# Performance work log

Hardware: AMD Instinct MI355X
Metric: run time of the kernel (lower is better)

## Reference

```python
import jax, jax.numpy as jnp
import numpy as np

EPS = 1e-5
KC = 256  # key_channels


def conv1x1(x, w):
    # x: [N,Cin,H,W], w: [Cout,Cin] -> [N,Cout,H,W]
    return jnp.einsum('nchw,oc->nohw', x, w)


def bn_relu(x, g, b, m, v):
    # eval-mode BatchNorm2d + ReLU, fused affine form
    inv = g / jnp.sqrt(v + EPS)
    return jax.nn.relu(x * inv[None, :, None, None] + (b - m * inv)[None, :, None, None])


def setup_inputs() -> dict:
    key = jax.random.key(0)
    ks = jax.random.split(key, 8)
    N, C, H, W, K = 8, 512, 128, 128, 19
    d = {
        'x': jax.random.normal(ks[0], (N, C, H, W), jnp.float32),
        'proxy': jax.random.normal(ks[1], (N, C, K, 1), jnp.float32),
        'w_p1': jax.random.normal(ks[2], (KC, C), jnp.float32) / np.sqrt(C),
        'w_p2': jax.random.normal(ks[3], (KC, KC), jnp.float32) / np.sqrt(KC),
        'w_o1': jax.random.normal(ks[4], (KC, C), jnp.float32) / np.sqrt(C),
        'w_o2': jax.random.normal(ks[5], (KC, KC), jnp.float32) / np.sqrt(KC),
        'w_d': jax.random.normal(ks[6], (KC, C), jnp.float32) / np.sqrt(C),
        'w_u': jax.random.normal(ks[7], (C, KC), jnp.float32) / np.sqrt(KC),
    }
    for pfx, ch in [('p1', KC), ('p2', KC), ('o1', KC), ('o2', KC), ('d', KC), ('u', C)]:
        d[f'{pfx}_g'] = jnp.ones((ch,), jnp.float32)
        d[f'{pfx}_b'] = jnp.zeros((ch,), jnp.float32)
        d[f'{pfx}_m'] = jnp.zeros((ch,), jnp.float32)
        d[f'{pfx}_v'] = jnp.ones((ch,), jnp.float32)
    return d


def reference(x, proxy, w_p1, p1_g, p1_b, p1_m, p1_v, w_p2, p2_g, p2_b, p2_m, p2_v,
              w_o1, o1_g, o1_b, o1_m, o1_v, w_o2, o2_g, o2_b, o2_m, o2_v,
              w_d, d_g, d_b, d_m, d_v, w_u, u_g, u_b, u_m, u_v):
    N, C, H, W = x.shape
    # f_pixel: conv1x1 -> BN+ReLU -> conv1x1 -> BN+ReLU
    q = bn_relu(conv1x1(bn_relu(conv1x1(x, w_p1), p1_g, p1_b, p1_m, p1_v), w_p2),
                p2_g, p2_b, p2_m, p2_v)                       # [N,KC,H,W]
    k = bn_relu(conv1x1(bn_relu(conv1x1(proxy, w_o1), o1_g, o1_b, o1_m, o1_v), w_o2),
                o2_g, o2_b, o2_m, o2_v)                       # [N,KC,K,1]
    v = bn_relu(conv1x1(proxy, w_d), d_g, d_b, d_m, d_v)      # [N,KC,K,1]

    query = q.reshape(N, KC, H * W).transpose(0, 2, 1)        # [N,HW,KC]
    keym = k.reshape(N, KC, -1)                               # [N,KC,K]
    value = v.reshape(N, KC, -1).transpose(0, 2, 1)           # [N,K,KC]

    sim = jnp.einsum('nlc,nck->nlk', query, keym) * (KC ** -0.5)  # [N,HW,K]
    sim = jax.nn.softmax(sim, axis=-1)
    context = jnp.einsum('nlk,nkc->nlc', sim, value)          # [N,HW,KC]
    context = context.transpose(0, 2, 1).reshape(N, KC, H, W)
    # f_up
    return bn_relu(conv1x1(context, w_u), u_g, u_b, u_m, u_v)  # [N,C,H,W]
```

## Files before the change

kernel.cpp:

```cpp
#include <hip/hip_runtime.h>

#define HW     16384
#define CIN    512
#define KCH    256
#define NKEY   19
#define NKP    32
#define NBATCH 8

typedef __attribute__((ext_vector_type(8))) short s16x8;
typedef __attribute__((ext_vector_type(4))) short s16x4;
typedef __attribute__((ext_vector_type(4))) float f32x4;

__device__ __forceinline__ short f2bf(float f) {
  __bf16 h = (__bf16)f;
  return __builtin_bit_cast(short, h);
}

__global__ __launch_bounds__(256) void kprepA(
    const float* __restrict__ proxy,
    const float* __restrict__ w_p1, const float* __restrict__ w_p2,
    const float* __restrict__ p1g, const float* __restrict__ p1b,
    const float* __restrict__ p1m, const float* __restrict__ p1v,
    const float* __restrict__ p2g, const float* __restrict__ p2b,
    const float* __restrict__ p2m, const float* __restrict__ p2v,
    const float* __restrict__ ug,  const float* __restrict__ ub,
    const float* __restrict__ um,  const float* __restrict__ uvv,
    const float* __restrict__ w_o1, const float* __restrict__ w_d,
    const float* __restrict__ o1g, const float* __restrict__ o1b,
    const float* __restrict__ o1m, const float* __restrict__ o1v,
    const float* __restrict__ dg,  const float* __restrict__ db,
    const float* __restrict__ dm,  const float* __restrict__ dv,
    short* __restrict__ W1L, short* __restrict__ W2L,
    float* __restrict__ b1, float* __restrict__ b2, float* __restrict__ bu,
    float* __restrict__ t_o1g, float* __restrict__ vmatg)
{
  __shared__ char PB[32 * 1024];
  const int tid = threadIdx.x;
  if (blockIdx.x < 772) {
    int t = blockIdx.x * 256 + tid;
    if (t < 131072) {
      int kf = t >> 13, rem = t & 8191, tt = rem >> 9, e512 = rem & 511;
      int l = e512 >> 3, e = e512 & 7;
      int m = tt * 16 + (l & 15);
      int kcol = kf * 32 + (l >> 4) * 8 + e;
      float inv = p1g[m] * rsqrtf(p1v[m] + 1e-5f);
      W1L[t] = f2bf(inv * w_p1[(size_t)m * CIN + kcol]);
    } else if (t < 196608) {
      int u = t - 131072;
      int kf = u >> 13, rem = u & 8191, tt = rem >> 9, e512 = rem & 511;
      int l = e512 >> 3, e = e512 & 7;
      int m = tt * 16 + (l & 15);
      int kcol = kf * 32 + (l >> 4) * 8 + e;
      float inv = p2g[m] * rsqrtf(p2v[m] + 1e-5f);
      W2L[u] = f2bf(inv * w_p2[(size_t)m * KCH + kcol]);
    } else if (t < 196608 + 256) {
      int o = t - 196608;
      float inv = p1g[o] * rsqrtf(p1v[o] + 1e-5f);
      b1[o] = p1b[o] - p1m[o] * inv;
    } else if (t < 196608 + 512) {
      int o = t - 196608 - 256;
      float inv = p2g[o] * rsqrtf(p2v[o] + 1e-5f);
      b2[o] = p2b[o] - p2m[o] * inv;
    } else if (t < 196608 + 1024) {
      int o = t - 196608 - 512;
      float inv = ug[o] * rsqrtf(uvv[o] + 1e-5f);
      bu[o] = ub[o] - um[o] * inv;
    }
    return;
  }
  int bid = blockIdx.x - 772;
  int sel = bid >> 5;
  int r5  = bid & 31;
  int n   = r5 >> 2;
  int mbase = (r5 & 3) << 6;

  for (int j = 0; j < 8; ++j) *(s16x8*)(PB + (tid + j * 256) * 16) = (s16x8)0;
  __syncthreads();
  const float* pn = proxy + (size_t)n * CIN * NKEY;
  for (int e = tid; e < CIN * NKEY; e += 256) {
    int c = e / NKEY, k = e - c * NKEY;
    *(short*)(PB + k * 1024 + ((c << 1) ^ ((k & 7) << 4))) = f2bf(pn[e]);
  }
  __syncthreads();

  const int w = tid >> 6, lane = tid & 63, g = lane >> 4, i = lane & 15;
  const float* W  = sel ? w_d : w_o1;
  const float* gg = sel ? dg : o1g;
  const float* bb = sel ? db : o1b;
  const float* mm = sel ? dm : o1m;
  const float* vv = sel ? dv : o1v;
  f32x4 acc2[2];
  acc2[0] = (f32x4)0.f; acc2[1] = (f32x4)0.f;
  const int arow = mbase + w * 16 + i;
#pragma unroll 1
  for (int kf = 0; kf < 16; ++kf) {
    const float* wp = W + (size_t)arow * CIN + kf * 32 + g * 8;
    f32x4 a0 = *(const f32x4*)wp, a1 = *(const f32x4*)(wp + 4);
    s16x8 af;
#pragma unroll
    for (int e = 0; e < 4; ++e) { af[e] = f2bf(a0[e]); af[e + 4] = f2bf(a1[e]); }
#pragma unroll
    for (int nj = 0; nj < 2; ++nj) {
      int key = nj * 16 + i;
      s16x8 bf = *(const s16x8*)(PB + key * 1024 + ((kf * 64 + g * 16) ^ ((key & 7) << 4)));
      acc2[nj] = __builtin_amdgcn_mfma_f32_16x16x32_bf16(af, bf, acc2[nj], 0, 0, 0);
    }
  }
  float* dst = (sel ? vmatg : t_o1g) + (size_t)n * 8192;
#pragma unroll
  for (int r = 0; r < 4; ++r) {
    int o = mbase + w * 16 + g * 4 + r;
    float inv = gg[o] * rsqrtf(vv[o] + 1e-5f);
    float beta = bb[o] - mm[o] * inv;
#pragma unroll
    for (int nj = 0; nj < 2; ++nj) {
      int key = nj * 16 + i;
      dst[key * 256 + o] = fmaxf(acc2[nj][r] * inv + beta, 0.f);
    }
  }
}

__global__ __launch_bounds__(256) void kprepB(
    const float* __restrict__ w_o2, const float* __restrict__ w_u,
    const float* __restrict__ o2g, const float* __restrict__ o2b,
    const float* __restrict__ o2m, const float* __restrict__ o2v,
    const float* __restrict__ ug,  const float* __restrict__ uvv,
    const float* __restrict__ t_o1g, const float* __restrict__ vmatg,
    short* __restrict__ KmL, short* __restrict__ WuL)
{
  __shared__ char TB[32 * 512];
  const int tid = threadIdx.x;
  const int isKm = (blockIdx.x < 32);
  int n, mbase;
  const float* src;
  if (isKm) { n = blockIdx.x >> 2; mbase = (blockIdx.x & 3) << 6; src = t_o1g; }
  else { int b2_ = blockIdx.x - 32; n = b2_ >> 3; mbase = (b2_ & 7) << 6; src = vmatg; }
  const float* sn = src + (size_t)n * 8192;
  for (int j = 0; j < 32; ++j) {
    int idx = tid + j * 256;
    int key = idx >> 8, o = idx & 255;
    *(short*)(TB + key * 512 + ((o << 1) ^ ((key & 7) << 4))) = f2bf(sn[idx]);
  }
  __syncthreads();

  const int w = tid >> 6, lane = tid & 63, g = lane >> 4, i = lane & 15;
  const float* W = isKm ? w_o2 : w_u;
  f32x4 acc2[2];
  acc2[0] = (f32x4)0.f; acc2[1] = (f32x4)0.f;
  const int arow = mbase + w * 16 + i;
#pragma unroll 1
  for (int kf = 0; kf < 8; ++kf) {
    const float* wp = W + (size_t)arow * KCH + kf * 32 + g * 8;
    f32x4 a0 = *(const f32x4*)wp, a1 = *(const f32x4*)(wp + 4);
    s16x8 af;
#pragma unroll
    for (int e = 0; e < 4; ++e) { af[e] = f2bf(a0[e]); af[e + 4] = f2bf(a1[e]); }
#pragma unroll
    for (int nj = 0; nj < 2; ++nj) {
      int key = nj * 16 + i;
      s16x8 bf = *(const s16x8*)(TB + key * 512 + ((kf * 64 + g * 16) ^ ((key & 7) << 4)));
      acc2[nj] = __builtin_amdgcn_mfma_f32_16x16x32_bf16(af, bf, acc2[nj], 0, 0, 0);
    }
  }
  if (isKm) {
    short* Kn = KmL + (size_t)n * 8192;
#pragma unroll
    for (int r = 0; r < 4; ++r) {
      int o2 = mbase + w * 16 + g * 4 + r;
      float inv = o2g[o2] * rsqrtf(o2v[o2] + 1e-5f);
      float beta = o2b[o2] - o2m[o2] * inv;
#pragma unroll
      for (int nj = 0; nj < 2; ++nj) {
        float val = fmaxf(acc2[nj][r] * inv + beta, 0.f) * 0.0625f;
        Kn[((o2 >> 5) * 2 + nj) * 512 + (((o2 >> 3) & 3) * 16 + i) * 8 + (o2 & 7)] = f2bf(val);
      }
    }
  } else {
    short* Wn = WuL + (size_t)n * 16384;
#pragma unroll
    for (int r = 0; r < 4; ++r) {
      int c = mbase + w * 16 + g * 4 + r;
      float inv = ug[c] * rsqrtf(uvv[c] + 1e-5f);
#pragma unroll
      for (int nj = 0; nj < 2; ++nj) {
        int key = nj * 16 + i;
        float val = acc2[nj][r] * inv;
        Wn[(c >> 4) * 512 + ((key >> 3) * 16 + (c & 15)) * 8 + (key & 7)] = f2bf(val);
      }
    }
  }
}

#define LOADCHUNK(R, ck) do { \
    const float* xp = xb + (size_t)((ck) * 64 + scb) * HW; \
    _Pragma("unroll") \
    for (int ii = 0; ii < 16; ++ii) (R)[ii] = xp[(size_t)ii * HW]; \
  } while (0)

#define WRITECHUNK(R, ck) do { \
    s16x8 h0, h1; \
    _Pragma("unroll") \
    for (int ii = 0; ii < 8; ++ii) { h0[ii] = f2bf((R)[ii]); h1[ii] = f2bf((R)[ii + 8]); } \
    char* wr_ = smem + ((ck) % 3) * 8192 + sp * 128; \
    *(s16x8*)(wr_ + (((scb << 1) +  0) ^ ssw)) = h0; \
    *(s16x8*)(wr_ + (((scb << 1) + 16) ^ ssw)) = h1; \
  } while (0)

#define MFMASTEP(ck) do { \
    const char* rb_ = smem + ((ck) % 3) * 8192; \
    _Pragma("unroll") \
    for (int ks = 0; ks < 2; ++ks) { \
      s16x8 af[4], bf[4]; \
      _Pragma("unroll") \
      for (int mi = 0; mi < 4; ++mi) \
        af[mi] = *(const s16x8*)(W1L + ((((ck) * 2 + ks) * 16 + (w * 4 + mi)) << 9) + (lane << 3)); \
      _Pragma("unroll") \
      for (int ni = 0; ni < 4; ++ni) { \
        int p_ = ni * 16 + i; \
        bf[ni] = *(const s16x8*)(rb_ + p_ * 128 + (((ks * 32 + g * 8) << 1) ^ ((p_ & 7) << 4))); \
      } \
      _Pragma("unroll") \
      for (int mi = 0; mi < 4; ++mi) \
        _Pragma("unroll") \
        for (int ni = 0; ni < 4; ++ni) \
          acc[mi][ni] = __builtin_amdgcn_mfma_f32_16x16x32_bf16(af[mi], bf[ni], acc[mi][ni], 0, 0, 0); \
    } \
  } while (0)

__global__ __launch_bounds__(256, 4) void k_main(
    const float* __restrict__ x,
    const short* __restrict__ W1L, const short* __restrict__ W2L,
    const short* __restrict__ KmL, const short* __restrict__ WuL,
    const float* __restrict__ b1, const float* __restrict__ b2,
    const float* __restrict__ bu,
    float* __restrict__ out)
{
  __shared__ char smem[32768];
  char* t1q = smem;

  const int tid  = threadIdx.x;
  const int w    = tid >> 6;
  const int lane = tid & 63;
  const int g    = lane >> 4;
  const int i    = lane & 15;
  const int n    = blockIdx.x >> 8;
  const int l0   = (blockIdx.x & 255) << 6;

  f32x4 acc[4][4];
#pragma unroll
  for (int a_ = 0; a_ < 4; ++a_)
#pragma unroll
    for (int b_ = 0; b_ < 4; ++b_) acc[a_][b_] = (f32x4)0.f;

  const int sp  = lane;
  const int scb = w << 4;
  const int ssw = (sp & 7) << 4;
  const float* xb = x + (size_t)n * CIN * HW + l0 + sp;

  float RA[16], RB[16];
  LOADCHUNK(RA, 0);
  LOADCHUNK(RB, 1);
  WRITECHUNK(RA, 0);
  __syncthreads();

#pragma unroll
  for (int cp = 0; cp < 4; ++cp) {
    const int cka = 2 * cp, ckb = 2 * cp + 1;
    if (cka + 2 < 8) LOADCHUNK(RA, cka + 2);
    WRITECHUNK(RB, ckb);
    MFMASTEP(cka);
    __syncthreads();
    if (ckb + 2 < 8) LOADCHUNK(RB, ckb + 2);
    if (ckb + 1 < 8) WRITECHUNK(RA, ckb + 1);
    MFMASTEP(ckb);
    __syncthreads();
  }

#pragma unroll
  for (int mi = 0; mi < 4; ++mi) {
    f32x4 bias = *(const f32x4*)(b1 + w * 64 + mi * 16 + g * 4);
#pragma unroll
    for (int ni = 0; ni < 4; ++ni) {
      int p = ni * 16 + i;
      s16x4 hh;
#pragma unroll
      for (int r = 0; r < 4; ++r) hh[r] = f2bf(fmaxf(acc[mi][ni][r] + bias[r], 0.f));
      *(s16x4*)(t1q + p * 512 + (((w * 64 + mi * 16 + g * 4) << 1) ^ ((p & 7) << 4))) = hh;
      acc[mi][ni] = (f32x4)0.f;
    }
  }
  __syncthreads();

#pragma unroll 2
  for (int ks = 0; ks < 8; ++ks) {
    s16x8 af[4], bf[4];
#pragma unroll
    for (int mi = 0; mi < 4; ++mi)
      af[mi] = *(const s16x8*)(W2L + (((ks * 16) + (w * 4 + mi)) << 9) + (lane << 3));
#pragma unroll
    for (int ni = 0; ni < 4; ++ni) {
      int p = ni * 16 + i;
      bf[ni] = *(const s16x8*)(t1q + p * 512 + (((ks * 32 + g * 8) << 1) ^ ((p & 7) << 4)));
    }
#pragma unroll
    for (int mi = 0; mi < 4; ++mi)
#pragma unroll
      for (int ni = 0; ni < 4; ++ni)
        acc[mi][ni] = __builtin_amdgcn_mfma_f32_16x16x32_bf16(af[mi], bf[ni], acc[mi][ni], 0, 0, 0);
  }
  __syncthreads();
#pragma unroll
  for (int mi = 0; mi < 4; ++mi) {
    f32x4 bias = *(const f32x4*)(b2 + w * 64 + mi * 16 + g * 4);
#pragma unroll
    for (int ni = 0; ni < 4; ++ni) {
      int p = ni * 16 + i;
      s16x4 hh;
#pragma unroll
      for (int r = 0; r < 4; ++r) hh[r] = f2bf(fmaxf(acc[mi][ni][r] + bias[r], 0.f));
      *(s16x4*)(t1q + p * 512 + (((w * 64 + mi * 16 + g * 4) << 1) ^ ((p & 7) << 4))) = hh;
    }
  }
  __syncthreads();

  f32x4 as_[2];
  as_[0] = (f32x4)0.f; as_[1] = (f32x4)0.f;
  const short* Kn = KmL + (size_t)n * 8192;
  const int ps = (w << 4) | i;
  const int psw = (ps & 7) << 4;
#pragma unroll
  for (int ks = 0; ks < 8; ++ks) {
    s16x8 bq = *(const s16x8*)(t1q + ps * 512 + (((ks * 32 + g * 8) << 1) ^ psw));
#pragma unroll
    for (int mi = 0; mi < 2; ++mi) {
      s16x8 ak = *(const s16x8*)(Kn + (((ks * 2 + mi)) << 9) + (lane << 3));
      as_[mi] = __builtin_amdgcn_mfma_f32_16x16x32_bf16(ak, bq, as_[mi], 0, 0, 0);
    }
  }
  float mx = -1e30f;
#pragma unroll
  for (int mi = 0; mi < 2; ++mi)
#pragma unroll
    for (int r = 0; r < 4; ++r) {
      int k = mi * 16 + g * 4 + r;
      if (k < NKEY) mx = fmaxf(mx, as_[mi][r]);
    }
  mx = fmaxf(mx, __shfl_xor(mx, 16, 64));
  mx = fmaxf(mx, __shfl_xor(mx, 32, 64));
  float e[2][4];
  float sum = 0.f;
#pragma unroll
  for (int mi = 0; mi < 2; ++mi)
#pragma unroll
    for (int r = 0; r < 4; ++r) {
      int k = mi * 16 + g * 4 + r;
      float t = (k < NKEY) ? __expf(as_[mi][r] - mx) : 0.f;
      e[mi][r] = t;
      sum += t;
    }
  sum += __shfl_xor(sum, 16, 64);
  sum += __shfl_xor(sum, 32, 64);
  float rs = 1.f / sum;
  __syncthreads();
  char* P = smem;
#pragma unroll
  for (int mi = 0; mi < 2; ++mi) {
    s16x4 hh;
#pragma unroll
    for (int r = 0; r < 4; ++r) hh[r] = f2bf(e[mi][r] * rs);
    *(s16x4*)(P + ps * 64 + (((mi * 16 + g * 4) << 1) ^ ((ps & 3) << 4))) = hh;
  }
  __syncthreads();

  s16x8 bP[4];
#pragma unroll
  for (int ni = 0; ni < 4; ++ni) {
    int p = ni * 16 + i;
    bP[ni] = *(const s16x8*)(P + p * 64 + ((g * 16) ^ ((p & 3) << 4)));
  }
  const short* Wn = WuL + (size_t)n * 16384;
  float* op = out + (size_t)n * CIN * HW + l0;
#pragma unroll
  for (int mi = 0; mi < 8; ++mi) {
    int row0 = w * 128 + mi * 16;
    s16x8 aU = *(const s16x8*)(Wn + ((w * 8 + mi) << 9) + (lane << 3));
    f32x4 bias = *(const f32x4*)(bu + row0 + g * 4);
#pragma unroll
    for (int ni = 0; ni < 4; ++ni) {
      f32x4 o4 = __builtin_amdgcn_mfma_f32_16x16x32_bf16(aU, bP[ni], bias, 0, 0, 0);
#pragma unroll
      for (int r = 0; r < 4; ++r)
        op[(size_t)(row0 + g * 4 + r) * HW + ni * 16 + i] = fmaxf(o4[r], 0.f);
    }
  }
}

extern "C" void kernel_launch(void* const* d_in, const int* in_sizes, int n_in,
                              void* d_out, int out_size, void* d_ws, size_t ws_size,
                              hipStream_t stream) {
  (void)in_sizes; (void)n_in; (void)out_size; (void)ws_size;
  const float* x     = (const float*)d_in[0];
  const float* proxy = (const float*)d_in[1];
  const float* w_p1  = (const float*)d_in[2];
  const float* w_p2  = (const float*)d_in[3];
  const float* w_o1  = (const float*)d_in[4];
  const float* w_o2  = (const float*)d_in[5];
  const float* w_d   = (const float*)d_in[6];
  const float* w_u   = (const float*)d_in[7];
  const float* p1g = (const float*)d_in[8],  *p1b = (const float*)d_in[9];
  const float* p1m = (const float*)d_in[10], *p1v = (const float*)d_in[11];
  const float* p2g = (const float*)d_in[12], *p2b = (const float*)d_in[13];
  const float* p2m = (const float*)d_in[14], *p2v = (const float*)d_in[15];
  const float* o1g = (const float*)d_in[16], *o1b = (const float*)d_in[17];
  const float* o1m = (const float*)d_in[18], *o1v = (const float*)d_in[19];
  const float* o2g = (const float*)d_in[20], *o2b = (const float*)d_in[21];
  const float* o2m = (const float*)d_in[22], *o2v = (const float*)d_in[23];
  const float* dg  = (const float*)d_in[24], *db  = (const float*)d_in[25];
  const float* dm  = (const float*)d_in[26], *dv  = (const float*)d_in[27];
  const float* ug  = (const float*)d_in[28], *ub  = (const float*)d_in[29];
  const float* um  = (const float*)d_in[30], *uv  = (const float*)d_in[31];

  char* ws = (char*)d_ws;
  short* W1L    = (short*)(ws + 0);
  short* W2L    = (short*)(ws + 262144);
  short* KmL    = (short*)(ws + 393216);
  short* WuL    = (short*)(ws + 524288);
  float* b1     = (float*)(ws + 786432);
  float* b2     = (float*)(ws + 787456);
  float* bu     = (float*)(ws + 788480);
  float* t_o1g  = (float*)(ws + 790528);
  float* vmatg  = (float*)(ws + 1052672);

  kprepA<<<836, 256, 0, stream>>>(proxy,
                                  w_p1, w_p2, p1g, p1b, p1m, p1v,
                                  p2g, p2b, p2m, p2v, ug, ub, um, uv,
                                  w_o1, w_d, o1g, o1b, o1m, o1v,
                                  dg, db, dm, dv,
                                  W1L, W2L, b1, b2, bu, t_o1g, vmatg);
  kprepB<<<96, 256, 0, stream>>>(w_o2, w_u, o2g, o2b, o2m, o2v, ug, uv,
                                 t_o1g, vmatg, KmL, WuL);
  k_main<<<2048, 256, 0, stream>>>(x, W1L, W2L, KmL, WuL, b1, b2, bu, (float*)d_out);
}
```

Measured before the change: 172.9 us.

## Stream x tiles into LDS via global_load_lds DMA and convert to bf16 on read

Replaces the register-staged load, bf16 convert and LDS write pipeline for the first projection GEMM with direct global-to-LDS DMA (global_load_lds, 16 bytes per lane) into a double-buffered fp32 tile using an XOR swizzle. The B fragments are now built from eight scalar fp32 LDS reads and converted to bf16 just before each MFMA. The loop is also collapsed into a non-unrolled single-chunk loop. The goal is to cut register usage and VALU staging work on the memory-bound x stream, at the cost of twice the LDS footprint per chunk, many more LDS read instructions, and each wave repeating the conversions.

```diff
diff --git a/kernel.cpp b/kernel.cpp
--- a/kernel.cpp
+++ b/kernel.cpp
@@ -191,23 +191,22 @@
   }
 }
 
-#define LOADCHUNK(R, ck) do { \
-    const float* xp = xb + (size_t)((ck) * 64 + scb) * HW; \
+#define DMACHUNK(ck) do { \
+    char* dst0 = smem + (((ck) & 1) << 14) + (w << 12); \
     _Pragma("unroll") \
-    for (int ii = 0; ii < 16; ++ii) (R)[ii] = xp[(size_t)ii * HW]; \
+    for (int t = 0; t < 4; ++t) { \
+      int chl = (w << 4) + (t << 2) + hi4; \
+      int js  = jq ^ ((chl >> 3) & 3); \
+      const float* srcp = xn + (size_t)((ck) * 64 + chl) * HW + (js << 2); \
+      __builtin_amdgcn_global_load_lds( \
+          (const __attribute__((address_space(1))) unsigned*)srcp, \
+          (__attribute__((address_space(3))) unsigned*)(dst0 + (t << 10)), \
+          16, 0, 0); \
+    } \
   } while (0)
 
-#define WRITECHUNK(R, ck) do { \
-    s16x8 h0, h1; \
-    _Pragma("unroll") \
-    for (int ii = 0; ii < 8; ++ii) { h0[ii] = f2bf((R)[ii]); h1[ii] = f2bf((R)[ii + 8]); } \
-    char* wr_ = smem + ((ck) % 3) * 8192 + sp * 128; \
-    *(s16x8*)(wr_ + (((scb << 1) +  0) ^ ssw)) = h0; \
-    *(s16x8*)(wr_ + (((scb << 1) + 16) ^ ssw)) = h1; \
-  } while (0)
-
-#define MFMASTEP(ck) do { \
-    const char* rb_ = smem + ((ck) % 3) * 8192; \
+#define MFMASTEP2(ck) do { \
+    const float* xsb = (const float*)(smem + (((ck) & 1) << 14)); \
     _Pragma("unroll") \
     for (int ks = 0; ks < 2; ++ks) { \
       s16x8 af[4], bf[4]; \
@@ -216,8 +215,14 @@
         af[mi] = *(const s16x8*)(W1L + ((((ck) * 2 + ks) * 16 + (w * 4 + mi)) << 9) + (lane << 3)); \
       _Pragma("unroll") \
       for (int ni = 0; ni < 4; ++ni) { \
-        int p_ = ni * 16 + i; \
-        bf[ni] = *(const s16x8*)(rb_ + p_ * 128 + (((ks * 32 + g * 8) << 1) ^ ((p_ & 7) << 4))); \
+        int px = ni * 16 + i; \
+        int col = ((((px >> 2) ^ g) << 2) | (px & 3)); \
+        const float* rp = xsb + (ks * 32 + g * 8) * 64 + col; \
+        float v[8]; \
+        _Pragma("unroll") \
+        for (int e = 0; e < 8; ++e) v[e] = rp[e * 64]; \
+        _Pragma("unroll") \
+        for (int e = 0; e < 8; ++e) bf[ni][e] = f2bf(v[e]); \
       } \
       _Pragma("unroll") \
       for (int mi = 0; mi < 4; ++mi) \
@@ -243,6 +248,8 @@
   const int lane = tid & 63;
   const int g    = lane >> 4;
   const int i    = lane & 15;
+  const int jq   = lane & 15;
+  const int hi4  = lane >> 4;
   const int n    = blockIdx.x >> 8;
   const int l0   = (blockIdx.x & 255) << 6;
 
@@ -252,27 +259,15 @@
 #pragma unroll
     for (int b_ = 0; b_ < 4; ++b_) acc[a_][b_] = (f32x4)0.f;
 
-  const int sp  = lane;
-  const int scb = w << 4;
-  const int ssw = (sp & 7) << 4;
-  const float* xb = x + (size_t)n * CIN * HW + l0 + sp;
-
-  float RA[16], RB[16];
-  LOADCHUNK(RA, 0);
-  LOADCHUNK(RB, 1);
-  WRITECHUNK(RA, 0);
-  __syncthreads();
-
-#pragma unroll
-  for (int cp = 0; cp < 4; ++cp) {
-    const int cka = 2 * cp, ckb = 2 * cp + 1;
-    if (cka + 2 < 8) LOADCHUNK(RA, cka + 2);
-    WRITECHUNK(RB, ckb);
-    MFMASTEP(cka);
-    __syncthreads();
-    if (ckb + 2 < 8) LOADCHUNK(RB, ckb + 2);
-    if (ckb + 1 < 8) WRITECHUNK(RA, ckb + 1);
-    MFMASTEP(ckb);
+  const float* xn = x + (size_t)n * CIN * HW + l0;
+
+  DMACHUNK(0);
+  __syncthreads();
+
+#pragma unroll 1
+  for (int ck = 0; ck < 8; ++ck) {
+    if (ck < 7) DMACHUNK(ck + 1);
+    MFMASTEP2(ck);
     __syncthreads();
   }
 
```

Measured after the change: 168.2 us. 1.03x faster.

## Vectorize x loads as float2 and stage output through LDS for float4 stores

Applied to the files above, without the earlier changes.

The first GEMM kernel now loads x with float2 per lane, covering two pixels by eight channels, and converts and writes them into the same swizzled LDS layout. The final projection epilogue no longer stores scalar floats straight from the MFMA layout. It writes results to a padded per-wave LDS tile and reads them back as float4, so each row store covers a wider contiguous span. This targets global memory transaction efficiency on the large input read and output write, at the cost of extra LDS traffic. The padded stride of 67 floats also leaves the float4 LDS reads unaligned to 16 bytes.

```diff
diff --git a/kernel.cpp b/kernel.cpp
--- a/kernel.cpp
+++ b/kernel.cpp
@@ -10,6 +10,7 @@
 typedef __attribute__((ext_vector_type(8))) short s16x8;
 typedef __attribute__((ext_vector_type(4))) short s16x4;
 typedef __attribute__((ext_vector_type(4))) float f32x4;
+typedef __attribute__((ext_vector_type(2))) float f32x2;
 
 __device__ __forceinline__ short f2bf(float f) {
   __bf16 h = (__bf16)f;
@@ -191,19 +192,22 @@
   }
 }
 
-#define LOADCHUNK(R, ck) do { \
-    const float* xp = xb + (size_t)((ck) * 64 + scb) * HW; \
+#define LOADCHUNK(R2, ck) do { \
+    const float* xp = xb2 + (size_t)((ck) * 64 + ch0) * HW; \
     _Pragma("unroll") \
-    for (int ii = 0; ii < 16; ++ii) (R)[ii] = xp[(size_t)ii * HW]; \
+    for (int c = 0; c < 8; ++c) (R2)[c] = *(const f32x2*)(xp + (size_t)c * HW); \
   } while (0)
 
-#define WRITECHUNK(R, ck) do { \
-    s16x8 h0, h1; \
+#define WRITECHUNK(R2, ck) do { \
+    char* wr_ = smem + ((ck) % 3) * 8192; \
     _Pragma("unroll") \
-    for (int ii = 0; ii < 8; ++ii) { h0[ii] = f2bf((R)[ii]); h1[ii] = f2bf((R)[ii + 8]); } \
-    char* wr_ = smem + ((ck) % 3) * 8192 + sp * 128; \
-    *(s16x8*)(wr_ + (((scb << 1) +  0) ^ ssw)) = h0; \
-    *(s16x8*)(wr_ + (((scb << 1) + 16) ^ ssw)) = h1; \
+    for (int p = 0; p < 2; ++p) { \
+      int px_ = pxp + p; \
+      s16x8 h; \
+      _Pragma("unroll") \
+      for (int c = 0; c < 8; ++c) h[c] = f2bf((R2)[c][p]); \
+      *(s16x8*)(wr_ + px_ * 128 + ((ch0 << 1) ^ ((px_ & 7) << 4))) = h; \
+    } \
   } while (0)
 
 #define MFMASTEP(ck) do { \
@@ -252,12 +256,11 @@
 #pragma unroll
     for (int b_ = 0; b_ < 4; ++b_) acc[a_][b_] = (f32x4)0.f;
 
-  const int sp  = lane;
-  const int scb = w << 4;
-  const int ssw = (sp & 7) << 4;
-  const float* xb = x + (size_t)n * CIN * HW + l0 + sp;
-
-  float RA[16], RB[16];
+  const int pxp = (lane & 31) << 1;
+  const int ch0 = (((lane >> 5) + (w << 1)) << 3);
+  const float* xb2 = x + (size_t)n * CIN * HW + l0 + pxp;
+
+  f32x2 RA[8], RB[8];
   LOADCHUNK(RA, 0);
   LOADCHUNK(RB, 1);
   WRITECHUNK(RA, 0);
@@ -380,6 +383,7 @@
   }
   const short* Wn = WuL + (size_t)n * 16384;
   float* op = out + (size_t)n * CIN * HW + l0;
+  float* Tb = (float*)(smem + 8192 + w * 4352);
 #pragma unroll
   for (int mi = 0; mi < 8; ++mi) {
     int row0 = w * 128 + mi * 16;
@@ -390,7 +394,13 @@
       f32x4 o4 = __builtin_amdgcn_mfma_f32_16x16x32_bf16(aU, bP[ni], bias, 0, 0, 0);
 #pragma unroll
       for (int r = 0; r < 4; ++r)
-        op[(size_t)(row0 + g * 4 + r) * HW + ni * 16 + i] = fmaxf(o4[r], 0.f);
+        Tb[(g * 4 + r) * 67 + ni * 16 + i] = fmaxf(o4[r], 0.f);
+    }
+#pragma unroll
+    for (int j = 0; j < 4; ++j) {
+      int rowr = j * 4 + g;
+      f32x4 v = *(const f32x4*)(Tb + rowr * 67 + i * 4);
+      *(f32x4*)(op + (size_t)(row0 + rowr) * HW + i * 4) = v;
     }
   }
 }
```

New measurement: 162.2 us (median of 3 runs). -6.2%, faster.
